# Kernel optimization log

Measured on AMD Instinct MI355X. Metric: run time of the kernel, lower is better.

Reference implementation:

```python
import jax, jax.numpy as jnp
import numpy as np

D_MODEL = 1024
NUM_HEADS = 16
HEAD_DIM = D_MODEL // NUM_HEADS
B, S = 4, 2048


def setup_inputs() -> dict:
    key = jax.random.key(0)
    ks = jax.random.split(key, 12)
    s = 1.0 / np.sqrt(D_MODEL)
    return {
        "inputs_q": jax.random.normal(ks[0], (B, S, D_MODEL), jnp.float32),
        "inputs_k": jax.random.normal(ks[1], (B, S, D_MODEL), jnp.float32),
        "inputs_v": jax.random.normal(ks[2], (B, S, D_MODEL), jnp.float32),
        "Wq": jax.random.normal(ks[3], (D_MODEL, D_MODEL), jnp.float32) * s,
        "bq": jax.random.normal(ks[4], (D_MODEL,), jnp.float32) * 0.01,
        "Wk": jax.random.normal(ks[5], (D_MODEL, D_MODEL), jnp.float32) * s,
        "bk": jax.random.normal(ks[6], (D_MODEL,), jnp.float32) * 0.01,
        "Wv": jax.random.normal(ks[7], (D_MODEL, D_MODEL), jnp.float32) * s,
        "bv": jax.random.normal(ks[8], (D_MODEL,), jnp.float32) * 0.01,
        "Wo": jax.random.normal(ks[9], (D_MODEL, D_MODEL), jnp.float32) * s,
        "bo": jax.random.normal(ks[10], (D_MODEL,), jnp.float32) * 0.01,
    }


def reference(inputs_q, inputs_k, inputs_v, Wq, bq, Wk, bk, Wv, bv, Wo, bo):
    b, s, _ = inputs_q.shape
    # linear projections
    q = inputs_q @ Wq + bq  # [b, s, d_model]
    k = inputs_k @ Wk + bk
    v = inputs_v @ Wv + bv
    # split heads: bsd -> bhsd
    q = q.reshape(b, s, NUM_HEADS, HEAD_DIM).transpose(0, 2, 1, 3)
    k = k.reshape(b, s, NUM_HEADS, HEAD_DIM).transpose(0, 2, 1, 3)
    v = v.reshape(b, s, NUM_HEADS, HEAD_DIM).transpose(0, 2, 1, 3)
    scale = 1.0 / jnp.sqrt(jnp.asarray(HEAD_DIM, q.dtype))
    scores = jnp.einsum('bhqd,bhkd->bhqk', q, k) * scale  # [b,h,s,s]
    # causal mask: position q attends to k <= q
    causal = jnp.tril(jnp.ones((s, s), dtype=bool))
    scores = jnp.where(causal[None, None], scores, jnp.asarray(-jnp.inf, scores.dtype))
    attn = jax.nn.softmax(scores, axis=-1)
    ctx = jnp.einsum('bhqk,bhkd->bhqd', attn, v)  # [b,h,s,hd]
    ctx = ctx.transpose(0, 2, 1, 3).reshape(b, s, D_MODEL)
    return ctx @ Wo + bo
```

## Files before the change

### kernel.cpp

```cpp
#include <hip/hip_runtime.h>
#include <math.h>
#include <type_traits>

typedef __bf16 bf16;
typedef __attribute__((ext_vector_type(8))) __bf16 bf16x8;
typedef __attribute__((ext_vector_type(4))) float f32x4;

#define SEQ 2048
#define DM 1024
#define NH 16
#define HD 64
#define BATCH 4

#define NEG_BIG (-1e30f)
#define SCALE_L2E 0.18033688011f

__device__ inline bf16x8 cvt_f32x8(const float* p) {
  f32x4 x0 = *(const f32x4*)p;
  f32x4 x1 = *(const f32x4*)(p + 4);
  bf16x8 r;
  r[0] = (bf16)x0[0]; r[1] = (bf16)x0[1]; r[2] = (bf16)x0[2]; r[3] = (bf16)x0[3];
  r[4] = (bf16)x1[0]; r[5] = (bf16)x1[1]; r[6] = (bf16)x1[2]; r[7] = (bf16)x1[3];
  return r;
}

__device__ inline void async_copy16(const bf16* g, bf16* l) {
  __builtin_amdgcn_global_load_lds(
      (const __attribute__((address_space(1))) unsigned int*)g,
      (__attribute__((address_space(3))) unsigned int*)l, 16, 0, 0);
}

__global__ __launch_bounds__(256) void cvt_kernel(const float* __restrict__ src,
                                                  bf16* __restrict__ dst) {
  size_t i = ((size_t)blockIdx.x * 256 + threadIdx.x) * 8;
  *(bf16x8*)(dst + i) = cvt_f32x8(src + i);
}

__global__ __launch_bounds__(256) void transpose_w_kernel(
    const float* __restrict__ Wq, const float* __restrict__ Wk,
    const float* __restrict__ Wv, const float* __restrict__ Wo,
    bf16* __restrict__ Tq, bf16* __restrict__ Tk,
    bf16* __restrict__ Tv, bf16* __restrict__ To) {
  __shared__ bf16 tile[64 * 66];
  int z = blockIdx.z;
  const float* src = (z == 0) ? Wq : (z == 1) ? Wk : (z == 2) ? Wv : Wo;
  bf16* dst = (z == 0) ? Tq : (z == 1) ? Tk : (z == 2) ? Tv : To;
  int n0 = blockIdx.x * 64, k0 = blockIdx.y * 64;
  int t = threadIdx.x;
  int c = t & 63, rr = t >> 6;
#pragma unroll
  for (int i = 0; i < 16; i++) {
    int k = i * 4 + rr;
    tile[k * 66 + c] = (bf16)src[(size_t)(k0 + k) * DM + n0 + c];
  }
  __syncthreads();
#pragma unroll
  for (int i = 0; i < 16; i++) {
    int n = i * 4 + rr;
    dst[(size_t)(n0 + n) * DM + k0 + c] = tile[c * 66 + n];
  }
}

__global__ __launch_bounds__(256) void transpose_v_kernel(
    const bf16* __restrict__ Vn, bf16* __restrict__ Vt) {
  __shared__ bf16 tile[64 * 66];
  int s0 = blockIdx.x * 64;
  int h = blockIdx.y, b = blockIdx.z;
  int t = threadIdx.x;
  int c = t & 63, rr = t >> 6;
#pragma unroll
  for (int i = 0; i < 16; i++) {
    int s = i * 4 + rr;
    tile[s * 66 + c] = Vn[((size_t)(b * SEQ + s0 + s)) * DM + h * HD + c];
  }
  __syncthreads();
#pragma unroll
  for (int i = 0; i < 16; i++) {
    int d = i * 4 + rr;
    Vt[((size_t)(b * NH + h) * HD + d) * SEQ + s0 + c] = tile[c * 66 + d];
  }
}

template <typename CT>
__global__ __launch_bounds__(256) void gemm_bias_kernel(
    const bf16* __restrict__ A, const bf16* __restrict__ Bt,
    const float* __restrict__ bias, CT* __restrict__ C) {
  __shared__ bf16 As[128 * 32];
  __shared__ bf16 Bs[128 * 32];
  int m0 = blockIdx.x * 128, n0 = blockIdx.y * 128;
  int t = threadIdx.x;
  int wave = t >> 6, lane = t & 63, lr = lane & 15, lq = lane >> 4;
  int wm = (wave & 1) * 64, wn = (wave >> 1) * 64;

  f32x4 acc[4][4];
#pragma unroll
  for (int i = 0; i < 4; i++)
#pragma unroll
    for (int j = 0; j < 4; j++) acc[i][j] = (f32x4){0.f, 0.f, 0.f, 0.f};

  int srow = wave * 32 + (lane >> 2);
  int skc = lane & 3;
  const bf16* gA0 = A + (size_t)(m0 + srow) * DM + skc * 8;
  const bf16* gA1 = gA0 + (size_t)16 * DM;
  const bf16* gB0 = Bt + (size_t)(n0 + srow) * DM + skc * 8;
  const bf16* gB1 = gB0 + (size_t)16 * DM;
  bf16* lA0 = &As[(wave * 128) * 8];
  bf16* lA1 = &As[(wave * 128 + 64) * 8];
  bf16* lB0 = &Bs[(wave * 128) * 8];
  bf16* lB1 = &Bs[(wave * 128 + 64) * 8];

  for (int k0 = 0; k0 < DM; k0 += 32) {
    async_copy16(gA0, lA0);
    async_copy16(gA1, lA1);
    async_copy16(gB0, lB0);
    async_copy16(gB1, lB1);
    gA0 += 32; gA1 += 32; gB0 += 32; gB1 += 32;
    __syncthreads();

    bf16x8 af[4], bfr[4];
#pragma unroll
    for (int i = 0; i < 4; i++)
      af[i] = *(const bf16x8*)&As[(wm + i * 16 + lr) * 32 + lq * 8];
#pragma unroll
    for (int j = 0; j < 4; j++)
      bfr[j] = *(const bf16x8*)&Bs[(wn + j * 16 + lr) * 32 + lq * 8];
#pragma unroll
    for (int i = 0; i < 4; i++)
#pragma unroll
      for (int j = 0; j < 4; j++)
        acc[i][j] = __builtin_amdgcn_mfma_f32_16x16x32_bf16(af[i], bfr[j],
                                                            acc[i][j], 0, 0, 0);
    __syncthreads();
  }

#pragma unroll
  for (int j = 0; j < 4; j++) {
    int col = n0 + wn + j * 16 + lr;
    float bv = bias[col];
#pragma unroll
    for (int i = 0; i < 4; i++) {
      int row = m0 + wm + i * 16 + lq * 4;
#pragma unroll
      for (int r = 0; r < 4; r++) {
        C[(size_t)(row + r) * DM + col] = (CT)(acc[i][j][r] + bv);
      }
    }
  }
}

__global__ __launch_bounds__(256, 2) void attention_kernel(
    const bf16* __restrict__ Q, const bf16* __restrict__ K,
    const bf16* __restrict__ Vt, bf16* __restrict__ ctx) {
  int h = blockIdx.y, b = blockIdx.z;
  int t = threadIdx.x, wave = t >> 6, lane = t & 63, lr = lane & 15,
      lq = lane >> 4;
  int p = blockIdx.x * 4 + wave;

  const bf16* Qb = Q + (size_t)b * SEQ * DM + h * HD;
  const bf16* Kb = K + (size_t)b * SEQ * DM + h * HD;
  const bf16* Vb = Vt + (size_t)(b * NH + h) * HD * SEQ;
  bf16* Cb = ctx + (size_t)b * SEQ * DM + h * HD;

#pragma unroll 1
  for (int pass = 0; pass < 2; pass++) {
    int tq = pass ? (63 - p) : p;
    int q0 = tq * 32;

    bf16x8 qf[2][2];
#pragma unroll
    for (int qi = 0; qi < 2; qi++)
#pragma unroll
      for (int ks = 0; ks < 2; ks++)
        qf[qi][ks] = *(const bf16x8*)&Qb[(size_t)(q0 + qi * 16 + lr) * DM +
                                         ks * 32 + lq * 8];

    f32x4 o[2][4];
    float m_st[2], l_st[2];
#pragma unroll
    for (int mi = 0; mi < 2; mi++) {
#pragma unroll
      for (int dj = 0; dj < 4; dj++) o[mi][dj] = (f32x4){0.f, 0.f, 0.f, 0.f};
      m_st[mi] = NEG_BIG;
      l_st[mi] = 0.f;
    }

    int kv_end = q0 + 32;
#pragma unroll 1
    for (int kv0 = 0; kv0 < kv_end; kv0 += 64) {
      bf16x8 kf[4][2];
#pragma unroll
      for (int kvt = 0; kvt < 4; kvt++)
#pragma unroll
        for (int ks = 0; ks < 2; ks++)
          kf[kvt][ks] = *(const bf16x8*)&Kb[(size_t)(kv0 + kvt * 16 + lr) * DM +
                                            ks * 32 + lq * 8];
      bf16x8 vf[4][2];
#pragma unroll
      for (int dj = 0; dj < 4; dj++)
#pragma unroll
        for (int ks2 = 0; ks2 < 2; ks2++)
          vf[dj][ks2] = *(const bf16x8*)&Vb[(size_t)(dj * 16 + lr) * SEQ + kv0 +
                                            ks2 * 32 + lq * 8];

      f32x4 s[4][2];
#pragma unroll
      for (int kvt = 0; kvt < 4; kvt++)
#pragma unroll
        for (int qi = 0; qi < 2; qi++) {
          f32x4 acc = (f32x4){0.f, 0.f, 0.f, 0.f};
          acc = __builtin_amdgcn_mfma_f32_16x16x32_bf16(kf[kvt][0], qf[qi][0],
                                                        acc, 0, 0, 0);
          acc = __builtin_amdgcn_mfma_f32_16x16x32_bf16(kf[kvt][1], qf[qi][1],
                                                        acc, 0, 0, 0);
          s[kvt][qi] = acc;
        }

      if (kv0 + 63 > q0) {
#pragma unroll
        for (int kvt = 0; kvt < 4; kvt++)
#pragma unroll
          for (int qi = 0; qi < 2; qi++)
#pragma unroll
            for (int r = 0; r < 4; r++) {
              int kv_g = kv0 + kvt * 16 + lq * 4 + r;
              int q_g = q0 + qi * 16 + lr;
              float v = s[kvt][qi][r] * SCALE_L2E;
              s[kvt][qi][r] = (kv_g > q_g) ? NEG_BIG : v;
            }
      } else {
#pragma unroll
        for (int kvt = 0; kvt < 4; kvt++)
#pragma unroll
          for (int qi = 0; qi < 2; qi++)
#pragma unroll
            for (int r = 0; r < 4; r++) s[kvt][qi][r] *= SCALE_L2E;
      }

      float alpha[2];
#pragma unroll
      for (int qi = 0; qi < 2; qi++) {
        float mx = s[0][qi][0];
#pragma unroll
        for (int kvt = 0; kvt < 4; kvt++)
#pragma unroll
          for (int r = 0; r < 4; r++) mx = fmaxf(mx, s[kvt][qi][r]);
        mx = fmaxf(mx, __shfl_xor(mx, 16));
        mx = fmaxf(mx, __shfl_xor(mx, 32));
        float mnew = fmaxf(m_st[qi], mx);
        alpha[qi] = exp2f(m_st[qi] - mnew);
        m_st[qi] = mnew;
        float rs = 0.f;
#pragma unroll
        for (int kvt = 0; kvt < 4; kvt++)
#pragma unroll
          for (int r = 0; r < 4; r++) {
            float pv = exp2f(s[kvt][qi][r] - mnew);
            s[kvt][qi][r] = pv;
            rs += pv;
          }
        rs += __shfl_xor(rs, 16);
        rs += __shfl_xor(rs, 32);
        l_st[qi] = l_st[qi] * alpha[qi] + rs;
      }

      float aT[2][4];
#pragma unroll
      for (int mi = 0; mi < 2; mi++)
#pragma unroll
        for (int r = 0; r < 4; r++) aT[mi][r] = __shfl(alpha[mi], lq * 4 + r);
#pragma unroll
      for (int mi = 0; mi < 2; mi++)
#pragma unroll
        for (int dj = 0; dj < 4; dj++)
#pragma unroll
          for (int r = 0; r < 4; r++) o[mi][dj][r] *= aT[mi][r];

      int src_base = (lq & 1) * 32 + lr;
      bool hi = (lq >> 1) != 0;
#pragma unroll
      for (int ks2 = 0; ks2 < 2; ks2++) {
        bf16x8 pf[2];
#pragma unroll
        for (int mi = 0; mi < 2; mi++) {
#pragma unroll
          for (int j = 0; j < 8; j++) {
            int src = src_base + (j >> 2) * 16;
            float v0 = __shfl(s[2 * ks2][mi][j & 3], src);
            float v1 = __shfl(s[2 * ks2 + 1][mi][j & 3], src);
            pf[mi][j] = (bf16)(hi ? v1 : v0);
          }
        }
#pragma unroll
        for (int dj = 0; dj < 4; dj++) {
          o[0][dj] = __builtin_amdgcn_mfma_f32_16x16x32_bf16(pf[0], vf[dj][ks2],
                                                             o[0][dj], 0, 0, 0);
          o[1][dj] = __builtin_amdgcn_mfma_f32_16x16x32_bf16(pf[1], vf[dj][ks2],
                                                             o[1][dj], 0, 0, 0);
        }
      }
    }

    float lT[2][4];
#pragma unroll
    for (int mi = 0; mi < 2; mi++)
#pragma unroll
      for (int r = 0; r < 4; r++)
        lT[mi][r] = 1.f / __shfl(l_st[mi], lq * 4 + r);
#pragma unroll
    for (int mi = 0; mi < 2; mi++)
#pragma unroll
      for (int r = 0; r < 4; r++) {
        int row = q0 + mi * 16 + lq * 4 + r;
#pragma unroll
        for (int dj = 0; dj < 4; dj++)
          Cb[(size_t)row * DM + dj * 16 + lr] = (bf16)(o[mi][dj][r] * lT[mi][r]);
      }
  }
}

extern "C" void kernel_launch(void* const* d_in, const int* in_sizes, int n_in,
                              void* d_out, int out_size, void* d_ws,
                              size_t ws_size, hipStream_t stream) {
  const float* iq = (const float*)d_in[0];
  const float* ik = (const float*)d_in[1];
  const float* iv = (const float*)d_in[2];
  const float* Wq = (const float*)d_in[3];
  const float* bq = (const float*)d_in[4];
  const float* Wk = (const float*)d_in[5];
  const float* bk = (const float*)d_in[6];
  const float* Wv = (const float*)d_in[7];
  const float* bv = (const float*)d_in[8];
  const float* Wo = (const float*)d_in[9];
  const float* bo = (const float*)d_in[10];

  char* ws = (char*)d_ws;
  const size_t MB = 1024 * 1024;
  bf16* Tq = (bf16*)(ws + 0 * MB);
  bf16* Tk = (bf16*)(ws + 2 * MB);
  bf16* Tv = (bf16*)(ws + 4 * MB);
  bf16* To = (bf16*)(ws + 6 * MB);
  bf16* Qp = (bf16*)(ws + 8 * MB);
  bf16* Kp = (bf16*)(ws + 24 * MB);
  bf16* Vp = (bf16*)(ws + 40 * MB);
  bf16* X = (bf16*)d_out;
  bf16* Vtp = (bf16*)d_out;
  bf16* Cx = Vp;

  transpose_w_kernel<<<dim3(16, 16, 4), 256, 0, stream>>>(Wq, Wk, Wv, Wo, Tq,
                                                          Tk, Tv, To);
  cvt_kernel<<<dim3(4096), 256, 0, stream>>>(iq, X);
  gemm_bias_kernel<bf16><<<dim3(64, 8), 256, 0, stream>>>(X, Tq, bq, Qp);
  cvt_kernel<<<dim3(4096), 256, 0, stream>>>(ik, X);
  gemm_bias_kernel<bf16><<<dim3(64, 8), 256, 0, stream>>>(X, Tk, bk, Kp);
  cvt_kernel<<<dim3(4096), 256, 0, stream>>>(iv, X);
  gemm_bias_kernel<bf16><<<dim3(64, 8), 256, 0, stream>>>(X, Tv, bv, Vp);
  transpose_v_kernel<<<dim3(32, 16, 4), 256, 0, stream>>>(Vp, Vtp);
  attention_kernel<<<dim3(8, 16, 4), 256, 0, stream>>>(Qp, Kp, Vtp, Cx);
  gemm_bias_kernel<float><<<dim3(64, 8), 256, 0, stream>>>(Cx, To, bo,
                                                           (float*)d_out);
}
```

Measured before the change: 402.1 us.

## Shrink attention query tile per wave to 16 rows and double grid

```diff
diff --git a/kernel.cpp b/kernel.cpp
--- a/kernel.cpp
+++ b/kernel.cpp
@@ -148,7 +148,7 @@
   }
 }
 
-__global__ __launch_bounds__(256, 2) void attention_kernel(
+__global__ __launch_bounds__(256, 4) void attention_kernel(
     const bf16* __restrict__ Q, const bf16* __restrict__ K,
     const bf16* __restrict__ Vt, bf16* __restrict__ ctx) {
   int h = blockIdx.y, b = blockIdx.z;
@@ -163,28 +163,20 @@
 
 #pragma unroll 1
   for (int pass = 0; pass < 2; pass++) {
-    int tq = pass ? (63 - p) : p;
-    int q0 = tq * 32;
-
-    bf16x8 qf[2][2];
-#pragma unroll
-    for (int qi = 0; qi < 2; qi++)
-#pragma unroll
-      for (int ks = 0; ks < 2; ks++)
-        qf[qi][ks] = *(const bf16x8*)&Qb[(size_t)(q0 + qi * 16 + lr) * DM +
-                                         ks * 32 + lq * 8];
-
-    f32x4 o[2][4];
-    float m_st[2], l_st[2];
-#pragma unroll
-    for (int mi = 0; mi < 2; mi++) {
-#pragma unroll
-      for (int dj = 0; dj < 4; dj++) o[mi][dj] = (f32x4){0.f, 0.f, 0.f, 0.f};
-      m_st[mi] = NEG_BIG;
-      l_st[mi] = 0.f;
-    }
-
-    int kv_end = q0 + 32;
+    int tq = pass ? (127 - p) : p;
+    int q0 = tq * 16;
+
+    bf16x8 qf[2];
+#pragma unroll
+    for (int ks = 0; ks < 2; ks++)
+      qf[ks] = *(const bf16x8*)&Qb[(size_t)(q0 + lr) * DM + ks * 32 + lq * 8];
+
+    f32x4 o[4];
+    float m_st = NEG_BIG, l_st = 0.f;
+#pragma unroll
+    for (int dj = 0; dj < 4; dj++) o[dj] = (f32x4){0.f, 0.f, 0.f, 0.f};
+
+    int kv_end = q0 + 16;
 #pragma unroll 1
     for (int kv0 = 0; kv0 < kv_end; kv0 += 64) {
       bf16x8 kf[4][2];
@@ -202,119 +194,94 @@
           vf[dj][ks2] = *(const bf16x8*)&Vb[(size_t)(dj * 16 + lr) * SEQ + kv0 +
                                             ks2 * 32 + lq * 8];
 
-      f32x4 s[4][2];
+      f32x4 s[4];
+#pragma unroll
+      for (int kvt = 0; kvt < 4; kvt++) {
+        f32x4 acc = (f32x4){0.f, 0.f, 0.f, 0.f};
+        acc = __builtin_amdgcn_mfma_f32_16x16x32_bf16(kf[kvt][0], qf[0], acc,
+                                                      0, 0, 0);
+        acc = __builtin_amdgcn_mfma_f32_16x16x32_bf16(kf[kvt][1], qf[1], acc,
+                                                      0, 0, 0);
+        s[kvt] = acc;
+      }
+
+      if (kv0 + 63 > q0) {
+#pragma unroll
+        for (int kvt = 0; kvt < 4; kvt++)
+#pragma unroll
+          for (int r = 0; r < 4; r++) {
+            int kv_g = kv0 + kvt * 16 + lq * 4 + r;
+            int q_g = q0 + lr;
+            float v = s[kvt][r] * SCALE_L2E;
+            s[kvt][r] = (kv_g > q_g) ? NEG_BIG : v;
+          }
+      } else {
+#pragma unroll
+        for (int kvt = 0; kvt < 4; kvt++)
+#pragma unroll
+          for (int r = 0; r < 4; r++) s[kvt][r] *= SCALE_L2E;
+      }
+
+      float mx = s[0][0];
 #pragma unroll
       for (int kvt = 0; kvt < 4; kvt++)
 #pragma unroll
-        for (int qi = 0; qi < 2; qi++) {
-          f32x4 acc = (f32x4){0.f, 0.f, 0.f, 0.f};
-          acc = __builtin_amdgcn_mfma_f32_16x16x32_bf16(kf[kvt][0], qf[qi][0],
-                                                        acc, 0, 0, 0);
-          acc = __builtin_amdgcn_mfma_f32_16x16x32_bf16(kf[kvt][1], qf[qi][1],
-                                                        acc, 0, 0, 0);
-          s[kvt][qi] = acc;
+        for (int r = 0; r < 4; r++) mx = fmaxf(mx, s[kvt][r]);
+      mx = fmaxf(mx, __shfl_xor(mx, 16));
+      mx = fmaxf(mx, __shfl_xor(mx, 32));
+      float mnew = fmaxf(m_st, mx);
+      float alpha = exp2f(m_st - mnew);
+      m_st = mnew;
+      float rs = 0.f;
+#pragma unroll
+      for (int kvt = 0; kvt < 4; kvt++)
+#pragma unroll
+        for (int r = 0; r < 4; r++) {
+          float pv = exp2f(s[kvt][r] - mnew);
+          s[kvt][r] = pv;
+          rs += pv;
         }
-
-      if (kv0 + 63 > q0) {
-#pragma unroll
-        for (int kvt = 0; kvt < 4; kvt++)
-#pragma unroll
-          for (int qi = 0; qi < 2; qi++)
-#pragma unroll
-            for (int r = 0; r < 4; r++) {
-              int kv_g = kv0 + kvt * 16 + lq * 4 + r;
-              int q_g = q0 + qi * 16 + lr;
-              float v = s[kvt][qi][r] * SCALE_L2E;
-              s[kvt][qi][r] = (kv_g > q_g) ? NEG_BIG : v;
-            }
-      } else {
-#pragma unroll
-        for (int kvt = 0; kvt < 4; kvt++)
-#pragma unroll
-          for (int qi = 0; qi < 2; qi++)
-#pragma unroll
-            for (int r = 0; r < 4; r++) s[kvt][qi][r] *= SCALE_L2E;
-      }
-
-      float alpha[2];
-#pragma unroll
-      for (int qi = 0; qi < 2; qi++) {
-        float mx = s[0][qi][0];
-#pragma unroll
-        for (int kvt = 0; kvt < 4; kvt++)
-#pragma unroll
-          for (int r = 0; r < 4; r++) mx = fmaxf(mx, s[kvt][qi][r]);
-        mx = fmaxf(mx, __shfl_xor(mx, 16));
-        mx = fmaxf(mx, __shfl_xor(mx, 32));
-        float mnew = fmaxf(m_st[qi], mx);
-        alpha[qi] = exp2f(m_st[qi] - mnew);
-        m_st[qi] = mnew;
-        float rs = 0.f;
-#pragma unroll
-        for (int kvt = 0; kvt < 4; kvt++)
-#pragma unroll
-          for (int r = 0; r < 4; r++) {
-            float pv = exp2f(s[kvt][qi][r] - mnew);
-            s[kvt][qi][r] = pv;
-            rs += pv;
-          }
-        rs += __shfl_xor(rs, 16);
-        rs += __shfl_xor(rs, 32);
-        l_st[qi] = l_st[qi] * alpha[qi] + rs;
-      }
-
-      float aT[2][4];
-#pragma unroll
-      for (int mi = 0; mi < 2; mi++)
-#pragma unroll
-        for (int r = 0; r < 4; r++) aT[mi][r] = __shfl(alpha[mi], lq * 4 + r);
-#pragma unroll
-      for (int mi = 0; mi < 2; mi++)
-#pragma unroll
-        for (int dj = 0; dj < 4; dj++)
-#pragma unroll
-          for (int r = 0; r < 4; r++) o[mi][dj][r] *= aT[mi][r];
+      rs += __shfl_xor(rs, 16);
+      rs += __shfl_xor(rs, 32);
+      l_st = l_st * alpha + rs;
+
+      float aT[4];
+#pragma unroll
+      for (int r = 0; r < 4; r++) aT[r] = __shfl(alpha, lq * 4 + r);
+#pragma unroll
+      for (int dj = 0; dj < 4; dj++)
+#pragma unroll
+        for (int r = 0; r < 4; r++) o[dj][r] *= aT[r];
 
       int src_base = (lq & 1) * 32 + lr;
       bool hi = (lq >> 1) != 0;
 #pragma unroll
       for (int ks2 = 0; ks2 < 2; ks2++) {
-        bf16x8 pf[2];
-#pragma unroll
-        for (int mi = 0; mi < 2; mi++) {
-#pragma unroll
-          for (int j = 0; j < 8; j++) {
-            int src = src_base + (j >> 2) * 16;
-            float v0 = __shfl(s[2 * ks2][mi][j & 3], src);
-            float v1 = __shfl(s[2 * ks2 + 1][mi][j & 3], src);
-            pf[mi][j] = (bf16)(hi ? v1 : v0);
-          }
+        bf16x8 pf;
+#pragma unroll
+        for (int j = 0; j < 8; j++) {
+          int src = src_base + (j >> 2) * 16;
+          float v0 = __shfl(s[2 * ks2][j & 3], src);
+          float v1 = __shfl(s[2 * ks2 + 1][j & 3], src);
+          pf[j] = (bf16)(hi ? v1 : v0);
         }
 #pragma unroll
-        for (int dj = 0; dj < 4; dj++) {
-          o[0][dj] = __builtin_amdgcn_mfma_f32_16x16x32_bf16(pf[0], vf[dj][ks2],
-                                                             o[0][dj], 0, 0, 0);
-          o[1][dj] = __builtin_amdgcn_mfma_f32_16x16x32_bf16(pf[1], vf[dj][ks2],
-                                                             o[1][dj], 0, 0, 0);
-        }
+        for (int dj = 0; dj < 4; dj++)
+          o[dj] = __builtin_amdgcn_mfma_f32_16x16x32_bf16(pf, vf[dj][ks2],
+                                                          o[dj], 0, 0, 0);
       }
     }
 
-    float lT[2][4];
-#pragma unroll
-    for (int mi = 0; mi < 2; mi++)
-#pragma unroll
-      for (int r = 0; r < 4; r++)
-        lT[mi][r] = 1.f / __shfl(l_st[mi], lq * 4 + r);
-#pragma unroll
-    for (int mi = 0; mi < 2; mi++)
-#pragma unroll
-      for (int r = 0; r < 4; r++) {
-        int row = q0 + mi * 16 + lq * 4 + r;
-#pragma unroll
-        for (int dj = 0; dj < 4; dj++)
-          Cb[(size_t)row * DM + dj * 16 + lr] = (bf16)(o[mi][dj][r] * lT[mi][r]);
-      }
+    float lT[4];
+#pragma unroll
+    for (int r = 0; r < 4; r++) lT[r] = 1.f / __shfl(l_st, lq * 4 + r);
+#pragma unroll
+    for (int r = 0; r < 4; r++) {
+      int row = q0 + lq * 4 + r;
+#pragma unroll
+      for (int dj = 0; dj < 4; dj++)
+        Cb[(size_t)row * DM + dj * 16 + lr] = (bf16)(o[dj][r] * lT[r]);
+    }
   }
 }
 
@@ -355,7 +322,7 @@
   cvt_kernel<<<dim3(4096), 256, 0, stream>>>(iv, X);
   gemm_bias_kernel<bf16><<<dim3(64, 8), 256, 0, stream>>>(X, Tv, bv, Vp);
   transpose_v_kernel<<<dim3(32, 16, 4), 256, 0, stream>>>(Vp, Vtp);
-  attention_kernel<<<dim3(8, 16, 4), 256, 0, stream>>>(Qp, Kp, Vtp, Cx);
+  attention_kernel<<<dim3(16, 16, 4), 256, 0, stream>>>(Qp, Kp, Vtp, Cx);
   gemm_bias_kernel<float><<<dim3(64, 8), 256, 0, stream>>>(Cx, To, bo,
                                                            (float*)d_out);
 }
```

After: 528.7 us. 31.5% more time.

## Double GEMM K-tile to 64 and use k-chunk-major LDS layout

Applied to the files above, without the earlier changes.

```diff
diff --git a/kernel.cpp b/kernel.cpp
--- a/kernel.cpp
+++ b/kernel.cpp
@@ -85,8 +85,8 @@
 __global__ __launch_bounds__(256) void gemm_bias_kernel(
     const bf16* __restrict__ A, const bf16* __restrict__ Bt,
     const float* __restrict__ bias, CT* __restrict__ C) {
-  __shared__ bf16 As[128 * 32];
-  __shared__ bf16 Bs[128 * 32];
+  __shared__ bf16 As[8 * 128 * 8];
+  __shared__ bf16 Bs[8 * 128 * 8];
   int m0 = blockIdx.x * 128, n0 = blockIdx.y * 128;
   int t = threadIdx.x;
   int wave = t >> 6, lane = t & 63, lr = lane & 15, lq = lane >> 4;
@@ -98,38 +98,54 @@
 #pragma unroll
     for (int j = 0; j < 4; j++) acc[i][j] = (f32x4){0.f, 0.f, 0.f, 0.f};
 
-  int srow = wave * 32 + (lane >> 2);
-  int skc = lane & 3;
-  const bf16* gA0 = A + (size_t)(m0 + srow) * DM + skc * 8;
-  const bf16* gA1 = gA0 + (size_t)16 * DM;
-  const bf16* gB0 = Bt + (size_t)(n0 + srow) * DM + skc * 8;
-  const bf16* gB1 = gB0 + (size_t)16 * DM;
-  bf16* lA0 = &As[(wave * 128) * 8];
-  bf16* lA1 = &As[(wave * 128 + 64) * 8];
-  bf16* lB0 = &Bs[(wave * 128) * 8];
-  bf16* lB1 = &Bs[(wave * 128 + 64) * 8];
-
-  for (int k0 = 0; k0 < DM; k0 += 32) {
-    async_copy16(gA0, lA0);
-    async_copy16(gA1, lA1);
-    async_copy16(gB0, lB0);
-    async_copy16(gB1, lB1);
-    gA0 += 32; gA1 += 32; gB0 += 32; gB1 += 32;
+  int kcl = wave, kch = wave + 4;
+  const bf16* gA_l0 = A + (size_t)(m0 + lane) * DM + kcl * 8;
+  const bf16* gA_l1 = A + (size_t)(m0 + 64 + lane) * DM + kcl * 8;
+  const bf16* gA_h0 = A + (size_t)(m0 + lane) * DM + kch * 8;
+  const bf16* gA_h1 = A + (size_t)(m0 + 64 + lane) * DM + kch * 8;
+  const bf16* gB_l0 = Bt + (size_t)(n0 + lane) * DM + kcl * 8;
+  const bf16* gB_l1 = Bt + (size_t)(n0 + 64 + lane) * DM + kcl * 8;
+  const bf16* gB_h0 = Bt + (size_t)(n0 + lane) * DM + kch * 8;
+  const bf16* gB_h1 = Bt + (size_t)(n0 + 64 + lane) * DM + kch * 8;
+  bf16* lA_l0 = &As[(kcl * 128 + 0) * 8];
+  bf16* lA_l1 = &As[(kcl * 128 + 64) * 8];
+  bf16* lA_h0 = &As[(kch * 128 + 0) * 8];
+  bf16* lA_h1 = &As[(kch * 128 + 64) * 8];
+  bf16* lB_l0 = &Bs[(kcl * 128 + 0) * 8];
+  bf16* lB_l1 = &Bs[(kcl * 128 + 64) * 8];
+  bf16* lB_h0 = &Bs[(kch * 128 + 0) * 8];
+  bf16* lB_h1 = &Bs[(kch * 128 + 64) * 8];
+
+  for (int k0 = 0; k0 < DM; k0 += 64) {
+    async_copy16(gA_l0, lA_l0);
+    async_copy16(gA_l1, lA_l1);
+    async_copy16(gA_h0, lA_h0);
+    async_copy16(gA_h1, lA_h1);
+    async_copy16(gB_l0, lB_l0);
+    async_copy16(gB_l1, lB_l1);
+    async_copy16(gB_h0, lB_h0);
+    async_copy16(gB_h1, lB_h1);
+    gA_l0 += 64; gA_l1 += 64; gA_h0 += 64; gA_h1 += 64;
+    gB_l0 += 64; gB_l1 += 64; gB_h0 += 64; gB_h1 += 64;
     __syncthreads();
 
-    bf16x8 af[4], bfr[4];
-#pragma unroll
-    for (int i = 0; i < 4; i++)
-      af[i] = *(const bf16x8*)&As[(wm + i * 16 + lr) * 32 + lq * 8];
-#pragma unroll
-    for (int j = 0; j < 4; j++)
-      bfr[j] = *(const bf16x8*)&Bs[(wn + j * 16 + lr) * 32 + lq * 8];
-#pragma unroll
-    for (int i = 0; i < 4; i++)
+#pragma unroll
+    for (int kb = 0; kb < 2; kb++) {
+      int kc = kb * 4 + lq;
+      bf16x8 af[4], bfr[4];
+#pragma unroll
+      for (int i = 0; i < 4; i++)
+        af[i] = *(const bf16x8*)&As[(kc * 128 + wm + i * 16 + lr) * 8];
 #pragma unroll
       for (int j = 0; j < 4; j++)
-        acc[i][j] = __builtin_amdgcn_mfma_f32_16x16x32_bf16(af[i], bfr[j],
-                                                            acc[i][j], 0, 0, 0);
+        bfr[j] = *(const bf16x8*)&Bs[(kc * 128 + wn + j * 16 + lr) * 8];
+#pragma unroll
+      for (int i = 0; i < 4; i++)
+#pragma unroll
+        for (int j = 0; j < 4; j++)
+          acc[i][j] = __builtin_amdgcn_mfma_f32_16x16x32_bf16(
+              af[i], bfr[j], acc[i][j], 0, 0, 0);
+    }
     __syncthreads();
   }
 
```

Result: slower. 443.8 us (+10.4%).

## Write Q/K/V projections in head-contiguous [b,h,s,d] layout for attention

Applied to the files above, without the earlier changes.

```diff
diff --git a/kernel.cpp b/kernel.cpp
--- a/kernel.cpp
+++ b/kernel.cpp
@@ -62,26 +62,28 @@
 }
 
 __global__ __launch_bounds__(256) void transpose_v_kernel(
-    const bf16* __restrict__ Vn, bf16* __restrict__ Vt) {
+    const bf16* __restrict__ Vc, bf16* __restrict__ Vt) {
   __shared__ bf16 tile[64 * 66];
   int s0 = blockIdx.x * 64;
-  int h = blockIdx.y, b = blockIdx.z;
+  int bh = blockIdx.y;
   int t = threadIdx.x;
   int c = t & 63, rr = t >> 6;
+  const bf16* src = Vc + (size_t)bh * SEQ * HD;
+  bf16* dst = Vt + (size_t)bh * HD * SEQ;
 #pragma unroll
   for (int i = 0; i < 16; i++) {
     int s = i * 4 + rr;
-    tile[s * 66 + c] = Vn[((size_t)(b * SEQ + s0 + s)) * DM + h * HD + c];
+    tile[s * 66 + c] = src[(size_t)(s0 + s) * HD + c];
   }
   __syncthreads();
 #pragma unroll
   for (int i = 0; i < 16; i++) {
     int d = i * 4 + rr;
-    Vt[((size_t)(b * NH + h) * HD + d) * SEQ + s0 + c] = tile[c * 66 + d];
-  }
-}
-
-template <typename CT>
+    dst[(size_t)d * SEQ + s0 + c] = tile[c * 66 + d];
+  }
+}
+
+template <typename CT, int MODE>
 __global__ __launch_bounds__(256) void gemm_bias_kernel(
     const bf16* __restrict__ A, const bf16* __restrict__ Bt,
     const float* __restrict__ bias, CT* __restrict__ C) {
@@ -139,25 +141,32 @@
     float bv = bias[col];
 #pragma unroll
     for (int i = 0; i < 4; i++) {
-      int row = m0 + wm + i * 16 + lq * 4;
+      int row0 = m0 + wm + i * 16 + lq * 4;
 #pragma unroll
       for (int r = 0; r < 4; r++) {
-        C[(size_t)(row + r) * DM + col] = (CT)(acc[i][j][r] + bv);
+        int row = row0 + r;
+        float v = acc[i][j][r] + bv;
+        if constexpr (MODE == 0) {
+          C[(size_t)row * DM + col] = (CT)v;
+        } else {
+          int b = row >> 11, s = row & 2047, h = col >> 6, d = col & 63;
+          C[((size_t)(b * NH + h) * SEQ + s) * HD + d] = (CT)v;
+        }
       }
     }
   }
 }
 
 __global__ __launch_bounds__(256, 2) void attention_kernel(
-    const bf16* __restrict__ Q, const bf16* __restrict__ K,
+    const bf16* __restrict__ Qc, const bf16* __restrict__ Kc,
     const bf16* __restrict__ Vt, bf16* __restrict__ ctx) {
   int h = blockIdx.y, b = blockIdx.z;
   int t = threadIdx.x, wave = t >> 6, lane = t & 63, lr = lane & 15,
       lq = lane >> 4;
   int p = blockIdx.x * 4 + wave;
 
-  const bf16* Qb = Q + (size_t)b * SEQ * DM + h * HD;
-  const bf16* Kb = K + (size_t)b * SEQ * DM + h * HD;
+  const bf16* Qb = Qc + (size_t)(b * NH + h) * SEQ * HD;
+  const bf16* Kb = Kc + (size_t)(b * NH + h) * SEQ * HD;
   const bf16* Vb = Vt + (size_t)(b * NH + h) * HD * SEQ;
   bf16* Cb = ctx + (size_t)b * SEQ * DM + h * HD;
 
@@ -171,7 +180,7 @@
     for (int qi = 0; qi < 2; qi++)
 #pragma unroll
       for (int ks = 0; ks < 2; ks++)
-        qf[qi][ks] = *(const bf16x8*)&Qb[(size_t)(q0 + qi * 16 + lr) * DM +
+        qf[qi][ks] = *(const bf16x8*)&Qb[(size_t)(q0 + qi * 16 + lr) * HD +
                                          ks * 32 + lq * 8];
 
     f32x4 o[2][4];
@@ -192,7 +201,7 @@
       for (int kvt = 0; kvt < 4; kvt++)
 #pragma unroll
         for (int ks = 0; ks < 2; ks++)
-          kf[kvt][ks] = *(const bf16x8*)&Kb[(size_t)(kv0 + kvt * 16 + lr) * DM +
+          kf[kvt][ks] = *(const bf16x8*)&Kb[(size_t)(kv0 + kvt * 16 + lr) * HD +
                                             ks * 32 + lq * 8];
       bf16x8 vf[4][2];
 #pragma unroll
@@ -339,23 +348,23 @@
   bf16* Tk = (bf16*)(ws + 2 * MB);
   bf16* Tv = (bf16*)(ws + 4 * MB);
   bf16* To = (bf16*)(ws + 6 * MB);
-  bf16* Qp = (bf16*)(ws + 8 * MB);
-  bf16* Kp = (bf16*)(ws + 24 * MB);
-  bf16* Vp = (bf16*)(ws + 40 * MB);
+  bf16* Qc = (bf16*)(ws + 8 * MB);
+  bf16* Kc = (bf16*)(ws + 24 * MB);
+  bf16* Vc = (bf16*)(ws + 40 * MB);
   bf16* X = (bf16*)d_out;
   bf16* Vtp = (bf16*)d_out;
-  bf16* Cx = Vp;
+  bf16* Cx = Vc;
 
   transpose_w_kernel<<<dim3(16, 16, 4), 256, 0, stream>>>(Wq, Wk, Wv, Wo, Tq,
                                                           Tk, Tv, To);
   cvt_kernel<<<dim3(4096), 256, 0, stream>>>(iq, X);
-  gemm_bias_kernel<bf16><<<dim3(64, 8), 256, 0, stream>>>(X, Tq, bq, Qp);
+  gemm_bias_kernel<bf16, 1><<<dim3(64, 8), 256, 0, stream>>>(X, Tq, bq, Qc);
   cvt_kernel<<<dim3(4096), 256, 0, stream>>>(ik, X);
-  gemm_bias_kernel<bf16><<<dim3(64, 8), 256, 0, stream>>>(X, Tk, bk, Kp);
+  gemm_bias_kernel<bf16, 1><<<dim3(64, 8), 256, 0, stream>>>(X, Tk, bk, Kc);
   cvt_kernel<<<dim3(4096), 256, 0, stream>>>(iv, X);
-  gemm_bias_kernel<bf16><<<dim3(64, 8), 256, 0, stream>>>(X, Tv, bv, Vp);
-  transpose_v_kernel<<<dim3(32, 16, 4), 256, 0, stream>>>(Vp, Vtp);
-  attention_kernel<<<dim3(8, 16, 4), 256, 0, stream>>>(Qp, Kp, Vtp, Cx);
-  gemm_bias_kernel<float><<<dim3(64, 8), 256, 0, stream>>>(Cx, To, bo,
-                                                           (float*)d_out);
-}
+  gemm_bias_kernel<bf16, 1><<<dim3(64, 8), 256, 0, stream>>>(X, Tv, bv, Vc);
+  transpose_v_kernel<<<dim3(32, 64), 256, 0, stream>>>(Vc, Vtp);
+  attention_kernel<<<dim3(8, 16, 4), 256, 0, stream>>>(Qc, Kc, Vtp, Cx);
+  gemm_bias_kernel<float, 0><<<dim3(64, 8), 256, 0, stream>>>(Cx, To, bo,
+                                                              (float*)d_out);
+}
```

Measured after the change: 400.5 us. No clear change (-0.4%).
